# Kernel tuning notes

Hardware: AMD Instinct MI355X
Metric: run time of the kernel (lower is better)

Reference implementation:

```python
import jax, jax.numpy as jnp
import numpy as np

B, T, C = 8, 2048, 512

def setup_inputs() -> dict:
    key = jax.random.key(0)
    ks = jax.random.split(key, 16)
    def n(k, shape, s=0.02):
        return jax.random.normal(k, shape, dtype=jnp.float32) * s
    inp = {
        'x_l': jax.random.normal(ks[0], (B, T, C), jnp.float32),
        'x_r': jax.random.normal(ks[1], (B, T, C), jnp.float32),
    }
    i = 2
    for name in ['lp1', 'rp1', 'lp2', 'rp2']:
        inp[name + '_w1'] = n(ks[i], (C, C))       # pointwise conv1d weight (out,in)
        inp[name + '_b1'] = jnp.zeros((C,), jnp.float32)
        inp[name + '_w2'] = n(ks[i + 1], (C, 3))   # depthwise conv k=3 weight per channel
        inp[name + '_b2'] = jnp.zeros((C,), jnp.float32)
        i += 2
    inp['lp3_w'] = n(ks[i], (C, C)); inp['lp3_b'] = jnp.zeros((C,), jnp.float32)
    inp['rp3_w'] = n(ks[i + 1], (C, C)); inp['rp3_b'] = jnp.zeros((C,), jnp.float32)
    return inp

def _proj(x, w1, b1, w2, b2):
    # x: (B,T,C). Pointwise conv1d (1x1) then depthwise conv1d k=3, pad=1 over T.
    h = jnp.einsum('btc,dc->btd', x, w1) + b1
    hp = jnp.pad(h, ((0, 0), (1, 1), (0, 0)))
    # cross-correlation: tap 0 -> t-1, tap 1 -> t, tap 2 -> t+1 (matches torch Conv1d)
    return hp[:, :-2, :] * w2[:, 0] + hp[:, 1:-1, :] * w2[:, 1] + hp[:, 2:, :] * w2[:, 2] + b2

def reference(x_l, x_r,
              lp1_w1, lp1_b1, lp1_w2, lp1_b2,
              rp1_w1, rp1_b1, rp1_w2, rp1_b2,
              lp2_w1, lp2_b1, lp2_w2, lp2_b2,
              rp2_w1, rp2_b1, rp2_w2, rp2_b2,
              lp3_w, lp3_b, rp3_w, rp3_b):
    scale = C ** (-0.5)
    Q_l = _proj(x_l, lp1_w1, lp1_b1, lp1_w2, lp1_b2)  # (B,T,C)
    Q_r = _proj(x_r, rp1_w1, rp1_b1, rp1_w2, rp1_b2)  # (B,T,C)
    V_l = _proj(x_l, lp2_w1, lp2_b1, lp2_w2, lp2_b2)  # (B,T,C)
    V_r = _proj(x_r, rp2_w1, rp2_b1, rp2_w2, rp2_b2)  # (B,T,C)
    attn = jnp.einsum('btc,bsc->bts', Q_l, Q_r) * scale  # shared (B,T,T) scores
    # r->l: softmax over r-positions (last axis)
    F_r2l = jnp.einsum('bts,bsc->btc', jax.nn.softmax(attn, axis=-1), V_r)
    # l->r: softmax of attn^T over its last axis == softmax over axis 1 of attn
    F_l2r = jnp.einsum('bts,btc->bsc', jax.nn.softmax(attn, axis=1), V_l)
    out_l = x_l + jnp.einsum('btc,dc->btd', F_r2l, lp3_w) + lp3_b
    out_r = x_r + jnp.einsum('btc,dc->btd', F_l2r, rp3_w) + rp3_b
    return (out_l, out_r)
```

## Files before the change

kernel.cpp:

```cpp
#include <hip/hip_runtime.h>
#include <stdint.h>

#define Bb 8
#define Tt 2048
#define Cc 512

typedef __attribute__((ext_vector_type(8))) short short8;
typedef __attribute__((ext_vector_type(4))) float f32x4;

#define SZE ((size_t)Bb * Tt * Cc)

__device__ __forceinline__ float b2f(short s) {
  unsigned int x = ((unsigned int)(unsigned short)s) << 16;
  return __builtin_bit_cast(float, x);
}
__device__ __forceinline__ short f2b(float f) {
  unsigned int x = __builtin_bit_cast(unsigned int, f);
  x += 0x7fffu + ((x >> 16) & 1u);
  return (short)(x >> 16);
}

template<int MODE>
__global__ __launch_bounds__(256, 2)
void gemm_bt(const void* __restrict__ Av, const void* __restrict__ Av2,
             const void* __restrict__ Bv, void* __restrict__ Cv,
             const float* __restrict__ bias,
             const float* __restrict__ resid, const float* __restrict__ resid2,
             int M, int N, int K,
             long long sA, long long sB, long long sC, float scale)
{
  __shared__ __align__(16) short ldsA[8 * 128 * 8];
  __shared__ __align__(16) short ldsB[8 * 128 * 8];
  const int tid  = threadIdx.x;
  const int lane = tid & 63;
  const int bm = blockIdx.y * 128;
  const int bn = blockIdx.x * 128;
  const long long zoA = (long long)blockIdx.z * sA;
  const long long zoB = (long long)blockIdx.z * sB;
  const long long zoC = (long long)blockIdx.z * sC;
  const void* Ause = Av;
  if constexpr (MODE == 0 || MODE == 3) {
    if (blockIdx.z) Ause = Av2;
  }
  const int wv = tid >> 6;
  const int wm = (wv >> 1) << 6;
  const int wn = (wv & 1) << 6;

  f32x4 zero4 = {0.f, 0.f, 0.f, 0.f};
  f32x4 acc[4][4];
#pragma unroll
  for (int i = 0; i < 4; ++i)
#pragma unroll
    for (int j = 0; j < 4; ++j)
      acc[i][j] = zero4;

  const int sm  = tid >> 3;
  const int skc = tid & 7;

  for (int k0 = 0; k0 < K; k0 += 64) {
#pragma unroll
    for (int r = 0; r < 4; ++r) {
      const int m = r * 32 + sm;
      short8 av, bv;
      if constexpr (MODE == 0) {
        const float* ap = (const float*)Ause + zoA + (size_t)(bm + m) * K + k0 + skc * 8;
        float4 f0 = *(const float4*)ap;
        float4 f1 = *(const float4*)(ap + 4);
        av[0] = f2b(f0.x); av[1] = f2b(f0.y); av[2] = f2b(f0.z); av[3] = f2b(f0.w);
        av[4] = f2b(f1.x); av[5] = f2b(f1.y); av[6] = f2b(f1.z); av[7] = f2b(f1.w);
      } else {
        av = *(const short8*)((const short*)Ause + zoA + (size_t)(bm + m) * K + k0 + skc * 8);
      }
      bv = *(const short8*)((const short*)Bv + zoB + (size_t)(bn + m) * K + k0 + skc * 8);
      const int di = ((skc << 7) + (m ^ skc)) << 3;
      *(short8*)&ldsA[di] = av;
      *(short8*)&ldsB[di] = bv;
    }
    __syncthreads();
#pragma unroll
    for (int kk = 0; kk < 2; ++kk) {
      const int kcr = (kk << 2) + (lane >> 4);
      short8 af[4], bfv[4];
#pragma unroll
      for (int i = 0; i < 4; ++i) {
        const int ma = wm + i * 16 + (lane & 15);
        const int nb = wn + i * 16 + (lane & 15);
        af[i]  = *(const short8*)&ldsA[((kcr << 7) + (ma ^ kcr)) << 3];
        bfv[i] = *(const short8*)&ldsB[((kcr << 7) + (nb ^ kcr)) << 3];
      }
#pragma unroll
      for (int i = 0; i < 4; ++i)
#pragma unroll
        for (int j = 0; j < 4; ++j)
          acc[i][j] = __builtin_amdgcn_mfma_f32_16x16x32_bf16(af[i], bfv[j], acc[i][j], 0, 0, 0);
    }
    __syncthreads();
  }

  const float* rp = resid;
  if constexpr (MODE == 3) {
    if (blockIdx.z) rp = resid2;
  }
#pragma unroll
  for (int i = 0; i < 4; ++i) {
    const int row0 = bm + wm + i * 16 + ((lane >> 4) << 2);
#pragma unroll
    for (int j = 0; j < 4; ++j) {
      const int n = bn + wn + j * 16 + (lane & 15);
      float badd = 0.f;
      if (MODE == 0 || MODE == 3) badd = bias[(size_t)blockIdx.z * N + n];
#pragma unroll
      for (int r = 0; r < 4; ++r) {
        float val = acc[i][j][r];
        const size_t off = (size_t)(row0 + r) * N + n;
        if (MODE == 1) val *= scale;
        if (MODE == 0) val += badd;
        if constexpr (MODE == 3) {
          val += badd + rp[off];
          ((float*)Cv)[zoC + off] = val;
        } else {
          ((short*)Cv)[zoC + off] = f2b(val);
        }
      }
    }
  }
}

__global__ __launch_bounds__(256)
void pack_all(const float* __restrict__ lw1a, const float* __restrict__ lw1b,
              const float* __restrict__ rw1a, const float* __restrict__ rw1b,
              const float* __restrict__ w3lf, const float* __restrict__ w3rf,
              const float* __restrict__ lb1a, const float* __restrict__ lb1b,
              const float* __restrict__ rb1a, const float* __restrict__ rb1b,
              const float* __restrict__ b3l, const float* __restrict__ b3r,
              short* __restrict__ Wl, short* __restrict__ Wr,
              short* __restrict__ W3l, short* __restrict__ W3r,
              float* __restrict__ BL, float* __restrict__ BR,
              float* __restrict__ B3)
{
  const int i = blockIdx.x * 256 + threadIdx.x;
  if (i < 524288) {
    Wl[i] = f2b(i < 262144 ? lw1a[i] : lw1b[i - 262144]);
  } else if (i < 1048576) {
    const int j = i - 524288;
    Wr[j] = f2b(j < 262144 ? rw1a[j] : rw1b[j - 262144]);
  } else if (i < 1310720) {
    W3l[i - 1048576] = f2b(w3lf[i - 1048576]);
  } else if (i < 1572864) {
    W3r[i - 1310720] = f2b(w3rf[i - 1310720]);
  } else if (i < 1573888) {
    const int j = i - 1572864;
    BL[j] = j < 512 ? lb1a[j] : lb1b[j - 512];
  } else if (i < 1574912) {
    const int j = i - 1573888;
    BR[j] = j < 512 ? rb1a[j] : rb1b[j - 512];
  } else if (i < 1575936) {
    const int j = i - 1574912;
    B3[j] = j < 512 ? b3l[j] : b3r[j - 512];
  }
}

__global__ __launch_bounds__(256)
void dw_kernel(const short* __restrict__ H, long long hStride,
               const float* __restrict__ w2a, const float* __restrict__ w2b,
               const float* __restrict__ b2a, const float* __restrict__ b2b,
               short* __restrict__ out, int colOff)
{
  const int dir = blockIdx.y;
  const short* Hd = H + (size_t)dir * hStride;
  const float* w2 = dir ? w2b : w2a;
  const float* b2 = dir ? b2b : b2a;
  short* outd = out + (size_t)dir * SZE;

  const int idx = blockIdx.x * 256 + threadIdx.x;
  const int c8 = idx & 63;
  const int bt = idx >> 6;
  const int t  = bt & (Tt - 1);
  const int c  = c8 << 3;
  const short* base = Hd + (size_t)bt * 1024 + colOff + c;
  short8 zz = {0, 0, 0, 0, 0, 0, 0, 0};
  short8 hm = zz, hp = zz;
  short8 h0 = *(const short8*)base;
  if (t > 0)      hm = *(const short8*)(base - 1024);
  if (t < Tt - 1) hp = *(const short8*)(base + 1024);
  short8 o;
#pragma unroll
  for (int j = 0; j < 8; ++j) {
    const int cj = c + j;
    float val = b2f(hm[j]) * w2[cj * 3 + 0]
              + b2f(h0[j]) * w2[cj * 3 + 1]
              + b2f(hp[j]) * w2[cj * 3 + 2]
              + b2[cj];
    o[j] = f2b(val);
  }
  *(short8*)(outd + (size_t)bt * Cc + c) = o;
}

__global__ __launch_bounds__(256)
void dwt_kernel(const short* __restrict__ H, long long hStride,
                const float* __restrict__ w2a, const float* __restrict__ w2b,
                const float* __restrict__ b2a, const float* __restrict__ b2b,
                short* __restrict__ outT, int colOff)
{
  const int dir = blockIdx.z >> 3;
  const int b   = blockIdx.z & 7;
  const short* Hd = H + (size_t)dir * hStride;
  const float* w2 = dir ? w2b : w2a;
  const float* b2 = dir ? b2b : b2a;
  short* outd = outT + (size_t)dir * SZE;

  const int c  = blockIdx.y * 64 + (threadIdx.x & 63);
  const int tb = blockIdx.x * 32 + (threadIdx.x >> 6) * 8;
  const short* base = Hd + ((size_t)b * Tt) * 1024 + colOff + c;
  float h[10];
#pragma unroll
  for (int i = 0; i < 10; ++i) {
    const int t = tb - 1 + i;
    h[i] = (t >= 0 && t < Tt) ? b2f(base[(size_t)t * 1024]) : 0.f;
  }
  const float w0 = w2[c * 3 + 0];
  const float w1 = w2[c * 3 + 1];
  const float wp = w2[c * 3 + 2];
  const float bb = b2[c];
  short8 o;
#pragma unroll
  for (int j = 0; j < 8; ++j)
    o[j] = f2b(h[j] * w0 + h[j + 1] * w1 + h[j + 2] * wp + bb);
  *(short8*)(outd + ((size_t)b * Cc + c) * Tt + tb) = o;
}

__global__ __launch_bounds__(256)
void pnorm_kernel(short* __restrict__ S)
{
  __shared__ float red[4];
  const size_t row = blockIdx.x;
  short8* p = (short8*)(S + row * (size_t)Tt) + threadIdx.x;
  const short8 v = *p;
  float x[8];
  float mx = -1e30f;
#pragma unroll
  for (int j = 0; j < 8; ++j) { x[j] = b2f(v[j]); mx = fmaxf(mx, x[j]); }
#pragma unroll
  for (int off = 32; off > 0; off >>= 1) mx = fmaxf(mx, __shfl_xor(mx, off, 64));
  const int wvi = threadIdx.x >> 6;
  if ((threadIdx.x & 63) == 0) red[wvi] = mx;
  __syncthreads();
  mx = fmaxf(fmaxf(red[0], red[1]), fmaxf(red[2], red[3]));
  __syncthreads();
  float e[8];
  float s = 0.f;
#pragma unroll
  for (int j = 0; j < 8; ++j) { e[j] = __expf(x[j] - mx); s += e[j]; }
#pragma unroll
  for (int off = 32; off > 0; off >>= 1) s += __shfl_xor(s, off, 64);
  if ((threadIdx.x & 63) == 0) red[wvi] = s;
  __syncthreads();
  const float inv = 1.f / (red[0] + red[1] + red[2] + red[3]);
  short8 o;
#pragma unroll
  for (int j = 0; j < 8; ++j) o[j] = f2b(e[j] * inv);
  *p = o;
}

extern "C" void kernel_launch(void* const* d_in, const int* in_sizes, int n_in,
                              void* d_out, int out_size, void* d_ws, size_t ws_size,
                              hipStream_t stream)
{
  const float* x_l    = (const float*)d_in[0];
  const float* x_r    = (const float*)d_in[1];
  const float* lp1_w1 = (const float*)d_in[2];
  const float* lp1_b1 = (const float*)d_in[3];
  const float* lp1_w2 = (const float*)d_in[4];
  const float* lp1_b2 = (const float*)d_in[5];
  const float* rp1_w1 = (const float*)d_in[6];
  const float* rp1_b1 = (const float*)d_in[7];
  const float* rp1_w2 = (const float*)d_in[8];
  const float* rp1_b2 = (const float*)d_in[9];
  const float* lp2_w1 = (const float*)d_in[10];
  const float* lp2_b1 = (const float*)d_in[11];
  const float* lp2_w2 = (const float*)d_in[12];
  const float* lp2_b2 = (const float*)d_in[13];
  const float* rp2_w1 = (const float*)d_in[14];
  const float* rp2_b1 = (const float*)d_in[15];
  const float* rp2_w2 = (const float*)d_in[16];
  const float* rp2_b2 = (const float*)d_in[17];
  const float* lp3_w  = (const float*)d_in[18];
  const float* lp3_b  = (const float*)d_in[19];
  const float* rp3_w  = (const float*)d_in[20];
  const float* rp3_b  = (const float*)d_in[21];

  short* ws = (short*)d_ws;
  const size_t SZ = SZE;
  short* Ql  = ws;
  short* Qr  = ws + SZ;
  short* VTl = ws + 2 * SZ;
  short* VTr = ws + 3 * SZ;
  short* Fb0 = ws + 4 * SZ;
  short* Sb  = ws + 5 * SZ;
  short* H   = Sb;

  const size_t W_PAIR = 524288, W_SING = 262144;
  const size_t tail_elems = 2 * W_PAIR + 2 * W_SING + 3 * 2048;
  const bool planA = ws_size >= 2 * (9 * SZ + tail_elems);
  const size_t tail = planA ? 9 * SZ : 7 * SZ;
  short* Wl  = ws + tail;
  short* Wr  = Wl + W_PAIR;
  short* W3l = Wr + W_PAIR;
  short* W3r = W3l + W_SING;
  float* BL  = (float*)(W3r + W_SING);
  float* BR  = BL + 1024;
  float* B3  = BR + 1024;

  float* out_l = (float*)d_out;

  const float scale = 0.04419417382415922f;
  const int MT = Bb * Tt;
  const long long sQ = (long long)Tt * Cc;
  const long long sS = (long long)Tt * Tt;

  dim3 blk(256);

  pack_all<<<6156, blk, 0, stream>>>(lp1_w1, lp2_w1, rp1_w1, rp2_w1, lp3_w, rp3_w,
                                     lp1_b1, lp2_b1, rp1_b1, rp2_b1, lp3_b, rp3_b,
                                     Wl, Wr, W3l, W3r, BL, BR, B3);

  if (planA) {
    gemm_bt<0><<<dim3(8, 128, 2), blk, 0, stream>>>(
        x_l, x_r, Wl, H, BL, nullptr, nullptr,
        MT, 1024, Cc, 0, (long long)W_PAIR, (long long)(2 * SZ), 1.f);
    dw_kernel <<<dim3(4096, 2), blk, 0, stream>>>(
        H, (long long)(2 * SZ), lp1_w2, rp1_w2, lp1_b2, rp1_b2, Ql, 0);
    dwt_kernel<<<dim3(Tt / 32, 8, 2 * Bb), blk, 0, stream>>>(
        H, (long long)(2 * SZ), lp2_w2, rp2_w2, lp2_b2, rp2_b2, VTl, 512);

    for (int dir = 0; dir < 2; ++dir) {
      const short* Qa = dir == 0 ? Ql : Qr;
      const short* Qb = dir == 0 ? Qr : Ql;
      const short* Vt = dir == 0 ? VTr : VTl;
      short* Fout     = dir == 0 ? Fb0 : Ql;

      gemm_bt<1><<<dim3(Tt / 128, Tt / 128, Bb), blk, 0, stream>>>(
          Qa, nullptr, Qb, Sb, nullptr, nullptr, nullptr,
          Tt, Tt, Cc, sQ, sQ, sS, scale);
      pnorm_kernel<<<Bb * Tt, blk, 0, stream>>>(Sb);
      gemm_bt<1><<<dim3(Cc / 128, Tt / 128, Bb), blk, 0, stream>>>(
          Sb, nullptr, Vt, Fout, nullptr, nullptr, nullptr,
          Tt, Cc, Tt, sS, sQ, sQ, 1.f);
    }
    gemm_bt<3><<<dim3(Cc / 128, MT / 128, 2), blk, 0, stream>>>(
        Fb0, Ql, W3l, d_out, B3, x_l, x_r,
        MT, Cc, Cc, 0, (long long)W_SING, (long long)SZ, 1.f);
  } else {
    const int nz = 4;
    gemm_bt<0><<<dim3(8, 128, 1), blk, 0, stream>>>(
        x_l, nullptr, Wl, H, BL, nullptr, nullptr, MT, 1024, Cc, 0, 0, 0, 1.f);
    dw_kernel <<<dim3(4096, 1), blk, 0, stream>>>(H, 0, lp1_w2, lp1_w2, lp1_b2, lp1_b2, Ql, 0);
    dwt_kernel<<<dim3(Tt / 32, 8, Bb), blk, 0, stream>>>(H, 0, lp2_w2, lp2_w2, lp2_b2, lp2_b2, VTl, 512);

    gemm_bt<0><<<dim3(8, 128, 1), blk, 0, stream>>>(
        x_r, nullptr, Wr, H, BR, nullptr, nullptr, MT, 1024, Cc, 0, 0, 0, 1.f);
    dw_kernel <<<dim3(4096, 1), blk, 0, stream>>>(H, 0, rp1_w2, rp1_w2, rp1_b2, rp1_b2, Qr, 0);
    dwt_kernel<<<dim3(Tt / 32, 8, Bb), blk, 0, stream>>>(H, 0, rp2_w2, rp2_w2, rp2_b2, rp2_b2, VTr, 512);

    for (int dir = 0; dir < 2; ++dir) {
      const short* Qa = dir == 0 ? Ql : Qr;
      const short* Qb = dir == 0 ? Qr : Ql;
      const short* Vt = dir == 0 ? VTr : VTl;
      const short* W3 = dir == 0 ? W3l : W3r;
      const float* b3 = B3 + dir * 512;
      const float* xr = dir == 0 ? x_l : x_r;
      float* outp     = dir == 0 ? out_l : out_l + SZ;

      for (int g = 0; g < 2; ++g) {
        const long long o = (long long)g * nz * sQ;
        gemm_bt<1><<<dim3(Tt / 128, Tt / 128, nz), blk, 0, stream>>>(
            Qa + o, nullptr, Qb + o, Sb, nullptr, nullptr, nullptr,
            Tt, Tt, Cc, sQ, sQ, sS, scale);
        pnorm_kernel<<<nz * Tt, blk, 0, stream>>>(Sb);
        gemm_bt<1><<<dim3(Cc / 128, Tt / 128, nz), blk, 0, stream>>>(
            Sb, nullptr, Vt + o, Fb0 + o, nullptr, nullptr, nullptr,
            Tt, Cc, Tt, sS, sQ, sQ, 1.f);
      }
      gemm_bt<3><<<dim3(Cc / 128, MT / 128, 1), blk, 0, stream>>>(
          Fb0, nullptr, W3, outp, b3, xr, nullptr, MT, Cc, Cc, 0, 0, 0, 1.f);
    }
  }

  (void)in_sizes; (void)n_in; (void)out_size;
}
```

Baseline: 516.6 us.

## Share one exp score matrix across both softmax directions, normalize after PV

Computes the QK^T scores once, applies exp without max subtraction in the GEMM epilogue, and writes both E and its transpose. Row and column sums are accumulated with atomics, and normalization moves into the PV GEMM epilogue. Both directions then run in one batched launch. This drops the separate pnorm kernels, the second score GEMM and the duplicated launches. It also adds an XCD-aware block remap. Skipping max subtraction risks overflow if scores grow large. The transpose writes and atomics add traffic, and the workspace-size fallback plan is removed.

```diff
diff --git a/kernel.cpp b/kernel.cpp
--- a/kernel.cpp
+++ b/kernel.cpp
@@ -6,6 +6,7 @@
 #define Cc 512
 
 typedef __attribute__((ext_vector_type(8))) short short8;
+typedef __attribute__((ext_vector_type(4))) short short4v;
 typedef __attribute__((ext_vector_type(4))) float f32x4;
 
 #define SZE ((size_t)Bb * Tt * Cc)
@@ -23,9 +24,11 @@
 template<int MODE>
 __global__ __launch_bounds__(256, 2)
 void gemm_bt(const void* __restrict__ Av, const void* __restrict__ Av2,
-             const void* __restrict__ Bv, void* __restrict__ Cv,
+             const void* __restrict__ Bv, const void* __restrict__ Bv2,
+             void* __restrict__ Cv, void* __restrict__ Cv2,
              const float* __restrict__ bias,
              const float* __restrict__ resid, const float* __restrict__ resid2,
+             short* __restrict__ ET, float* __restrict__ sumR, float* __restrict__ sumC,
              int M, int N, int K,
              long long sA, long long sB, long long sC, float scale)
 {
@@ -33,15 +36,37 @@
   __shared__ __align__(16) short ldsB[8 * 128 * 8];
   const int tid  = threadIdx.x;
   const int lane = tid & 63;
-  const int bm = blockIdx.y * 128;
-  const int bn = blockIdx.x * 128;
-  const long long zoA = (long long)blockIdx.z * sA;
-  const long long zoB = (long long)blockIdx.z * sB;
-  const long long zoC = (long long)blockIdx.z * sC;
+
+  int bxi = blockIdx.x, byi = blockIdx.y, bzi = blockIdx.z;
+  const int gx = gridDim.x, gy = gridDim.y;
+  if ((gy & 7) == 0) {
+    int l = bxi + gx * (byi + gy * bzi);
+    const int xcd = l & 7;
+    int loc = l >> 3;
+    const int ych = gy >> 3;
+    bxi = loc % gx;  loc /= gx;
+    byi = xcd * ych + (loc % ych);
+    bzi = loc / ych;
+  }
+
+  const int bm = byi * 128;
+  const int bn = bxi * 128;
+  int dir = 0, zz = bzi;
+  if constexpr (MODE == 2) { dir = bzi >> 3; zz = bzi & 7; }
+  const long long zoA = (long long)zz * sA;
+  const long long zoB = (long long)zz * sB;
+  const long long zoC = (long long)zz * sC;
   const void* Ause = Av;
+  const void* Buse = Bv;
+  void* Cuse = Cv;
+  const float* rp = resid;
   if constexpr (MODE == 0 || MODE == 3) {
-    if (blockIdx.z) Ause = Av2;
-  }
+    if (zz) { Ause = Av2; rp = resid2; }
+  }
+  if constexpr (MODE == 2) {
+    if (dir) { Ause = Av2; Buse = Bv2; Cuse = Cv2; }
+  }
+
   const int wv = tid >> 6;
   const int wm = (wv >> 1) << 6;
   const int wn = (wv & 1) << 6;
@@ -71,7 +96,7 @@
       } else {
         av = *(const short8*)((const short*)Ause + zoA + (size_t)(bm + m) * K + k0 + skc * 8);
       }
-      bv = *(const short8*)((const short*)Bv + zoB + (size_t)(bn + m) * K + k0 + skc * 8);
+      bv = *(const short8*)((const short*)Buse + zoB + (size_t)(bn + m) * K + k0 + skc * 8);
       const int di = ((skc << 7) + (m ^ skc)) << 3;
       *(short8*)&ldsA[di] = av;
       *(short8*)&ldsB[di] = bv;
@@ -97,33 +122,92 @@
     __syncthreads();
   }
 
-  const float* rp = resid;
-  if constexpr (MODE == 3) {
-    if (blockIdx.z) rp = resid2;
-  }
-#pragma unroll
-  for (int i = 0; i < 4; ++i) {
-    const int row0 = bm + wm + i * 16 + ((lane >> 4) << 2);
+  if constexpr (MODE == 4) {
+#pragma unroll
+    for (int i = 0; i < 4; ++i)
+#pragma unroll
+      for (int j = 0; j < 4; ++j)
+#pragma unroll
+        for (int r = 0; r < 4; ++r)
+          acc[i][j][r] = __expf(acc[i][j][r] * scale);
+
+#pragma unroll
+    for (int i = 0; i < 4; ++i) {
+      const int row0 = bm + wm + i * 16 + ((lane >> 4) << 2);
+#pragma unroll
+      for (int j = 0; j < 4; ++j) {
+        const int n = bn + wn + j * 16 + (lane & 15);
+        short4v t;
+#pragma unroll
+        for (int r = 0; r < 4; ++r) t[r] = f2b(acc[i][j][r]);
+#pragma unroll
+        for (int r = 0; r < 4; ++r)
+          ((short*)Cv)[zoC + (size_t)(row0 + r) * N + n] = t[r];
+        *(short4v*)(ET + zoC + (size_t)n * M + row0) = t;
+      }
+    }
+#pragma unroll
+    for (int i = 0; i < 4; ++i) {
+      const int row0 = bm + wm + i * 16 + ((lane >> 4) << 2);
+#pragma unroll
+      for (int r = 0; r < 4; ++r) {
+        float p = acc[i][0][r] + acc[i][1][r] + acc[i][2][r] + acc[i][3][r];
+#pragma unroll
+        for (int o = 1; o < 16; o <<= 1) p += __shfl_xor(p, o, 64);
+        if ((lane & 15) == 0)
+          unsafeAtomicAdd(&sumR[(size_t)zz * M + row0 + r], p);
+      }
+    }
 #pragma unroll
     for (int j = 0; j < 4; ++j) {
       const int n = bn + wn + j * 16 + (lane & 15);
-      float badd = 0.f;
-      if (MODE == 0 || MODE == 3) badd = bias[(size_t)blockIdx.z * N + n];
+      float q = 0.f;
+#pragma unroll
+      for (int i = 0; i < 4; ++i)
+#pragma unroll
+        for (int r = 0; r < 4; ++r) q += acc[i][j][r];
+      q += __shfl_xor(q, 16, 64);
+      q += __shfl_xor(q, 32, 64);
+      if (lane < 16)
+        unsafeAtomicAdd(&sumC[(size_t)zz * N + n], q);
+    }
+  } else if constexpr (MODE == 2) {
+    const float* sums = dir ? sumC : sumR;
+#pragma unroll
+    for (int i = 0; i < 4; ++i) {
+      const int row0 = bm + wm + i * 16 + ((lane >> 4) << 2);
 #pragma unroll
       for (int r = 0; r < 4; ++r) {
-        float val = acc[i][j][r];
-        const size_t off = (size_t)(row0 + r) * N + n;
-        if (MODE == 1) val *= scale;
-        if (MODE == 0) val += badd;
-        if constexpr (MODE == 3) {
-          val += badd + rp[off];
-          ((float*)Cv)[zoC + off] = val;
-        } else {
-          ((short*)Cv)[zoC + off] = f2b(val);
+        const float iv = 1.0f / sums[(size_t)zz * M + row0 + r];
+#pragma unroll
+        for (int j = 0; j < 4; ++j) {
+          const int n = bn + wn + j * 16 + (lane & 15);
+          ((short*)Cuse)[zoC + (size_t)(row0 + r) * N + n] = f2b(acc[i][j][r] * iv);
         }
       }
     }
-  }
+  } else {
+#pragma unroll
+    for (int i = 0; i < 4; ++i) {
+      const int row0 = bm + wm + i * 16 + ((lane >> 4) << 2);
+#pragma unroll
+      for (int j = 0; j < 4; ++j) {
+        const int n = bn + wn + j * 16 + (lane & 15);
+        const float badd = bias[(size_t)zz * N + n];
+#pragma unroll
+        for (int r = 0; r < 4; ++r) {
+          float val = acc[i][j][r] + badd;
+          const size_t off = (size_t)(row0 + r) * N + n;
+          if constexpr (MODE == 3) {
+            ((float*)Cv)[zoC + off] = val + rp[off];
+          } else {
+            ((short*)Cv)[zoC + off] = f2b(val);
+          }
+        }
+      }
+    }
+  }
+  (void)scale; (void)ET; (void)sumR; (void)sumC; (void)Cuse; (void)rp;
 }
 
 __global__ __launch_bounds__(256)
@@ -136,7 +220,7 @@
               short* __restrict__ Wl, short* __restrict__ Wr,
               short* __restrict__ W3l, short* __restrict__ W3r,
               float* __restrict__ BL, float* __restrict__ BR,
-              float* __restrict__ B3)
+              float* __restrict__ B3, float* __restrict__ SUM)
 {
   const int i = blockIdx.x * 256 + threadIdx.x;
   if (i < 524288) {
@@ -157,6 +241,8 @@
   } else if (i < 1575936) {
     const int j = i - 1574912;
     B3[j] = j < 512 ? b3l[j] : b3r[j - 512];
+  } else if (i < 1608704) {
+    SUM[i - 1575936] = 0.f;
   }
 }
 
@@ -229,39 +315,6 @@
   *(short8*)(outd + ((size_t)b * Cc + c) * Tt + tb) = o;
 }
 
-__global__ __launch_bounds__(256)
-void pnorm_kernel(short* __restrict__ S)
-{
-  __shared__ float red[4];
-  const size_t row = blockIdx.x;
-  short8* p = (short8*)(S + row * (size_t)Tt) + threadIdx.x;
-  const short8 v = *p;
-  float x[8];
-  float mx = -1e30f;
-#pragma unroll
-  for (int j = 0; j < 8; ++j) { x[j] = b2f(v[j]); mx = fmaxf(mx, x[j]); }
-#pragma unroll
-  for (int off = 32; off > 0; off >>= 1) mx = fmaxf(mx, __shfl_xor(mx, off, 64));
-  const int wvi = threadIdx.x >> 6;
-  if ((threadIdx.x & 63) == 0) red[wvi] = mx;
-  __syncthreads();
-  mx = fmaxf(fmaxf(red[0], red[1]), fmaxf(red[2], red[3]));
-  __syncthreads();
-  float e[8];
-  float s = 0.f;
-#pragma unroll
-  for (int j = 0; j < 8; ++j) { e[j] = __expf(x[j] - mx); s += e[j]; }
-#pragma unroll
-  for (int off = 32; off > 0; off >>= 1) s += __shfl_xor(s, off, 64);
-  if ((threadIdx.x & 63) == 0) red[wvi] = s;
-  __syncthreads();
-  const float inv = 1.f / (red[0] + red[1] + red[2] + red[3]);
-  short8 o;
-#pragma unroll
-  for (int j = 0; j < 8; ++j) o[j] = f2b(e[j] * inv);
-  *p = o;
-}
-
 extern "C" void kernel_launch(void* const* d_in, const int* in_sizes, int n_in,
                               void* d_out, int out_size, void* d_ws, size_t ws_size,
                               hipStream_t stream)
@@ -269,21 +322,21 @@
   const float* x_l    = (const float*)d_in[0];
   const float* x_r    = (const float*)d_in[1];
   const float* lp1_w1 = (const float*)d_in[2];
-  const float* lp1_b1 = (const float*)d_in[3];
   const float* lp1_w2 = (const float*)d_in[4];
   const float* lp1_b2 = (const float*)d_in[5];
   const float* rp1_w1 = (const float*)d_in[6];
-  const float* rp1_b1 = (const float*)d_in[7];
   const float* rp1_w2 = (const float*)d_in[8];
   const float* rp1_b2 = (const float*)d_in[9];
   const float* lp2_w1 = (const float*)d_in[10];
-  const float* lp2_b1 = (const float*)d_in[11];
   const float* lp2_w2 = (const float*)d_in[12];
   const float* lp2_b2 = (const float*)d_in[13];
   const float* rp2_w1 = (const float*)d_in[14];
-  const float* rp2_b1 = (const float*)d_in[15];
   const float* rp2_w2 = (const float*)d_in[16];
   const float* rp2_b2 = (const float*)d_in[17];
+  const float* lp1_b1 = (const float*)d_in[3];
+  const float* rp1_b1 = (const float*)d_in[7];
+  const float* lp2_b1 = (const float*)d_in[11];
+  const float* rp2_b1 = (const float*)d_in[15];
   const float* lp3_w  = (const float*)d_in[18];
   const float* lp3_b  = (const float*)d_in[19];
   const float* rp3_w  = (const float*)d_in[20];
@@ -295,23 +348,22 @@
   short* Qr  = ws + SZ;
   short* VTl = ws + 2 * SZ;
   short* VTr = ws + 3 * SZ;
-  short* Fb0 = ws + 4 * SZ;
-  short* Sb  = ws + 5 * SZ;
-  short* H   = Sb;
+  short* E   = ws + 4 * SZ;
+  short* ETb = ws + 8 * SZ;
+  short* H   = E;
+  short* Fb0 = Qr;
+  short* Fb1 = Ql;
 
   const size_t W_PAIR = 524288, W_SING = 262144;
-  const size_t tail_elems = 2 * W_PAIR + 2 * W_SING + 3 * 2048;
-  const bool planA = ws_size >= 2 * (9 * SZ + tail_elems);
-  const size_t tail = planA ? 9 * SZ : 7 * SZ;
-  short* Wl  = ws + tail;
+  short* Wl  = ws + 12 * SZ;
   short* Wr  = Wl + W_PAIR;
   short* W3l = Wr + W_PAIR;
   short* W3r = W3l + W_SING;
   float* BL  = (float*)(W3r + W_SING);
   float* BR  = BL + 1024;
   float* B3  = BR + 1024;
-
-  float* out_l = (float*)d_out;
+  float* SUMR = B3 + 1024;
+  float* SUMC = SUMR + 16384;
 
   const float scale = 0.04419417382415922f;
   const int MT = Bb * Tt;
@@ -320,71 +372,33 @@
 
   dim3 blk(256);
 
-  pack_all<<<6156, blk, 0, stream>>>(lp1_w1, lp2_w1, rp1_w1, rp2_w1, lp3_w, rp3_w,
+  pack_all<<<6284, blk, 0, stream>>>(lp1_w1, lp2_w1, rp1_w1, rp2_w1, lp3_w, rp3_w,
                                      lp1_b1, lp2_b1, rp1_b1, rp2_b1, lp3_b, rp3_b,
-                                     Wl, Wr, W3l, W3r, BL, BR, B3);
-
-  if (planA) {
-    gemm_bt<0><<<dim3(8, 128, 2), blk, 0, stream>>>(
-        x_l, x_r, Wl, H, BL, nullptr, nullptr,
-        MT, 1024, Cc, 0, (long long)W_PAIR, (long long)(2 * SZ), 1.f);
-    dw_kernel <<<dim3(4096, 2), blk, 0, stream>>>(
-        H, (long long)(2 * SZ), lp1_w2, rp1_w2, lp1_b2, rp1_b2, Ql, 0);
-    dwt_kernel<<<dim3(Tt / 32, 8, 2 * Bb), blk, 0, stream>>>(
-        H, (long long)(2 * SZ), lp2_w2, rp2_w2, lp2_b2, rp2_b2, VTl, 512);
-
-    for (int dir = 0; dir < 2; ++dir) {
-      const short* Qa = dir == 0 ? Ql : Qr;
-      const short* Qb = dir == 0 ? Qr : Ql;
-      const short* Vt = dir == 0 ? VTr : VTl;
-      short* Fout     = dir == 0 ? Fb0 : Ql;
-
-      gemm_bt<1><<<dim3(Tt / 128, Tt / 128, Bb), blk, 0, stream>>>(
-          Qa, nullptr, Qb, Sb, nullptr, nullptr, nullptr,
-          Tt, Tt, Cc, sQ, sQ, sS, scale);
-      pnorm_kernel<<<Bb * Tt, blk, 0, stream>>>(Sb);
-      gemm_bt<1><<<dim3(Cc / 128, Tt / 128, Bb), blk, 0, stream>>>(
-          Sb, nullptr, Vt, Fout, nullptr, nullptr, nullptr,
-          Tt, Cc, Tt, sS, sQ, sQ, 1.f);
-    }
-    gemm_bt<3><<<dim3(Cc / 128, MT / 128, 2), blk, 0, stream>>>(
-        Fb0, Ql, W3l, d_out, B3, x_l, x_r,
-        MT, Cc, Cc, 0, (long long)W_SING, (long long)SZ, 1.f);
-  } else {
-    const int nz = 4;
-    gemm_bt<0><<<dim3(8, 128, 1), blk, 0, stream>>>(
-        x_l, nullptr, Wl, H, BL, nullptr, nullptr, MT, 1024, Cc, 0, 0, 0, 1.f);
-    dw_kernel <<<dim3(4096, 1), blk, 0, stream>>>(H, 0, lp1_w2, lp1_w2, lp1_b2, lp1_b2, Ql, 0);
-    dwt_kernel<<<dim3(Tt / 32, 8, Bb), blk, 0, stream>>>(H, 0, lp2_w2, lp2_w2, lp2_b2, lp2_b2, VTl, 512);
-
-    gemm_bt<0><<<dim3(8, 128, 1), blk, 0, stream>>>(
-        x_r, nullptr, Wr, H, BR, nullptr, nullptr, MT, 1024, Cc, 0, 0, 0, 1.f);
-    dw_kernel <<<dim3(4096, 1), blk, 0, stream>>>(H, 0, rp1_w2, rp1_w2, rp1_b2, rp1_b2, Qr, 0);
-    dwt_kernel<<<dim3(Tt / 32, 8, Bb), blk, 0, stream>>>(H, 0, rp2_w2, rp2_w2, rp2_b2, rp2_b2, VTr, 512);
-
-    for (int dir = 0; dir < 2; ++dir) {
-      const short* Qa = dir == 0 ? Ql : Qr;
-      const short* Qb = dir == 0 ? Qr : Ql;
-      const short* Vt = dir == 0 ? VTr : VTl;
-      const short* W3 = dir == 0 ? W3l : W3r;
-      const float* b3 = B3 + dir * 512;
-      const float* xr = dir == 0 ? x_l : x_r;
-      float* outp     = dir == 0 ? out_l : out_l + SZ;
-
-      for (int g = 0; g < 2; ++g) {
-        const long long o = (long long)g * nz * sQ;
-        gemm_bt<1><<<dim3(Tt / 128, Tt / 128, nz), blk, 0, stream>>>(
-            Qa + o, nullptr, Qb + o, Sb, nullptr, nullptr, nullptr,
-            Tt, Tt, Cc, sQ, sQ, sS, scale);
-        pnorm_kernel<<<nz * Tt, blk, 0, stream>>>(Sb);
-        gemm_bt<1><<<dim3(Cc / 128, Tt / 128, nz), blk, 0, stream>>>(
-            Sb, nullptr, Vt + o, Fb0 + o, nullptr, nullptr, nullptr,
-            Tt, Cc, Tt, sS, sQ, sQ, 1.f);
-      }
-      gemm_bt<3><<<dim3(Cc / 128, MT / 128, 1), blk, 0, stream>>>(
-          Fb0, nullptr, W3, outp, b3, xr, nullptr, MT, Cc, Cc, 0, 0, 0, 1.f);
-    }
-  }
-
-  (void)in_sizes; (void)n_in; (void)out_size;
-}
+                                     Wl, Wr, W3l, W3r, BL, BR, B3, SUMR);
+
+  gemm_bt<0><<<dim3(8, 128, 2), blk, 0, stream>>>(
+      x_l, x_r, Wl, nullptr, H, nullptr, BL, nullptr, nullptr,
+      nullptr, nullptr, nullptr,
+      MT, 1024, Cc, 0, (long long)W_PAIR, (long long)(2 * SZ), 1.f);
+  dw_kernel <<<dim3(4096, 2), blk, 0, stream>>>(
+      H, (long long)(2 * SZ), lp1_w2, rp1_w2, lp1_b2, rp1_b2, Ql, 0);
+  dwt_kernel<<<dim3(Tt / 32, 8, 2 * Bb), blk, 0, stream>>>(
+      H, (long long)(2 * SZ), lp2_w2, rp2_w2, lp2_b2, rp2_b2, VTl, 512);
+
+  gemm_bt<4><<<dim3(Tt / 128, Tt / 128, Bb), blk, 0, stream>>>(
+      Ql, nullptr, Qr, nullptr, E, nullptr, nullptr, nullptr, nullptr,
+      ETb, SUMR, SUMC,
+      Tt, Tt, Cc, sQ, sQ, sS, scale);
+
+  gemm_bt<2><<<dim3(Cc / 128, Tt / 128, 2 * Bb), blk, 0, stream>>>(
+      E, ETb, VTr, VTl, Fb0, Fb1, nullptr, nullptr, nullptr,
+      nullptr, SUMR, SUMC,
+      Tt, Cc, Tt, sS, sQ, sQ, 1.f);
+
+  gemm_bt<3><<<dim3(Cc / 128, MT / 128, 2), blk, 0, stream>>>(
+      Fb0, Fb1, W3l, nullptr, d_out, nullptr, B3, x_l, x_r,
+      nullptr, nullptr, nullptr,
+      MT, Cc, Cc, 0, (long long)W_SING, (long long)SZ, 1.f);
+
+  (void)in_sizes; (void)n_in; (void)out_size; (void)ws_size;
+}
```

New measurement: 439.8 us. 1.17x faster.
